# Performance work log

Hardware: AMD Instinct MI355X
Metric: run time of the kernel (lower is better)

## Reference

```python
import jax, jax.numpy as jnp
import numpy as np

E = 200000      # n_edges
IN = 128        # input_nf
HID = 32        # hidden_nf
H = 4           # att_heads
OUT = 128       # output_nf
MAXK = 16       # MAX_K neighbor slots


def setup_inputs() -> dict:
    key = jax.random.key(0)
    ks = jax.random.split(key, 12)
    Z = jax.random.normal(ks[0], (E, IN), dtype=jnp.float32)
    idx = jax.random.randint(ks[1], (E, 2, MAXK), 0, E)
    red = jax.random.uniform(ks[2], (E, 1, MAXK)) < 0.15
    klist = jnp.where(red, -1, idx).astype(jnp.int64)
    s = 0.05  # xavier-ish scale
    Wq = jax.random.normal(ks[3], (H, HID, IN), dtype=jnp.float32) * s
    Wk = jax.random.normal(ks[4], (H, HID, IN), dtype=jnp.float32) * s
    Wv = jax.random.normal(ks[5], (H, HID, IN), dtype=jnp.float32) * s
    Wb = jax.random.normal(ks[6], (H, 1, IN), dtype=jnp.float32) * s
    Wg = jax.random.normal(ks[7], (H, HID, IN), dtype=jnp.float32) * s
    bg = jnp.zeros((H, HID), dtype=jnp.float32)
    Wout = jax.random.normal(ks[8], (OUT, H * HID), dtype=jnp.float32) * s
    bout = jnp.zeros((OUT,), dtype=jnp.float32)
    return {"Z": Z, "klist": klist, "Wq": Wq, "Wk": Wk, "Wv": Wv,
            "Wb": Wb, "Wg": Wg, "bg": bg, "Wout": Wout, "bout": bout}


def reference(Z, klist, Wq, Wk, Wv, Wb, Wg, bg, Wout, bout):
    idx_i, idx_j = klist[:, 0], klist[:, 1]          # (E, K)
    red = idx_i == -1
    valid = (~red).astype(Z.dtype)[..., None]        # (E, K, 1)
    ii = jnp.where(red, 0, idx_i)
    jj = jnp.where(red, 0, idx_j)
    scale = 1.0 / np.sqrt(HID)
    outs = []
    for h in range(H):  # att_heads: small fixed loop over structurally distinct heads
        q = Z @ Wq[h].T                              # (E, HID)
        k = Z @ Wk[h].T
        v = Z @ Wv[h].T
        b = (Z @ Wb[h].T)[:, 0]                      # (E,)
        g = jax.nn.sigmoid(Z @ Wg[h].T + bg[h])      # (E, HID)
        tri_k = jnp.take(k, ii, axis=0) * valid      # (E, K, HID), redundant slots zeroed
        tri_v = jnp.take(v, ii, axis=0) * valid
        tri_b = jnp.take(b, jj, axis=0) * valid[..., 0]  # (E, K)
        scores = scale * jnp.einsum('eh,ekh->ek', q, tri_k) + tri_b
        alpha = jax.nn.softmax(scores, axis=1)       # (E, K)
        att = jnp.einsum('ek,ekh->eh', alpha, tri_v) # (E, HID)
        outs.append(g * att)
    out = jnp.concatenate(outs, axis=-1) @ Wout.T + bout  # (E, OUT)
    # dropout is identity in eval mode
    return out
```

## Files before the change

kernel.cpp:

```cpp
#include <hip/hip_runtime.h>
#include <hip/hip_bf16.h>
#include <stdint.h>

#define EDGES 200000
#define INF   128
#define HID   32
#define NHEAD 4
#define OUTF  128
#define MAXK  16

#define NPAD  528

#define XPAD  136

typedef unsigned short u16;
typedef __attribute__((ext_vector_type(8))) short bf16x8;
typedef __attribute__((ext_vector_type(4))) float f32x4;

__device__ __forceinline__ u16 f2bf(float f) {
  union { float f; uint32_t u; } v; v.f = f;
  uint32_t u = v.u;
  return (u16)((u + 0x7FFFu + ((u >> 16) & 1u)) >> 16);
}
__device__ __forceinline__ float bflo(uint32_t p) {
  union { uint32_t u; float f; } v; v.u = p << 16;
  return v.f;
}
__device__ __forceinline__ float bfhi(uint32_t p) {
  union { uint32_t u; float f; } v; v.u = p & 0xFFFF0000u;
  return v.f;
}

__device__ __forceinline__ uint32_t cvtpk_bf16(float lo, float hi) {
  float2 t; t.x = lo; t.y = hi;
  __hip_bfloat162 h = __float22bfloat162_rn(t);
  uint32_t u;
  __builtin_memcpy(&u, &h, 4);
  return u;
}
__device__ __forceinline__ bf16x8 pack8(float4 f0, float4 f1) {
  union { uint32_t u[4]; bf16x8 v; } r;
  r.u[0] = cvtpk_bf16(f0.x, f0.y);
  r.u[1] = cvtpk_bf16(f0.z, f0.w);
  r.u[2] = cvtpk_bf16(f1.x, f1.y);
  r.u[3] = cvtpk_bf16(f1.z, f1.w);
  return r.v;
}
__device__ __forceinline__ float sigm(float x) {
  return 1.0f / (1.0f + __expf(-x));
}

template <int CTRL>
__device__ __forceinline__ float dpp_add(float x) {
  int y = __builtin_amdgcn_update_dpp(0, __builtin_bit_cast(int, x),
                                      CTRL, 0xF, 0xF, true);
  return x + __builtin_bit_cast(float, y);
}
__device__ __forceinline__ float row16_sum(float x) {
  x = dpp_add<0xB1>(x);
  x = dpp_add<0x4E>(x);
  x = dpp_add<0x141>(x);
  x = dpp_add<0x140>(x);
  return x;
}

struct AccPair { f32x4 a, b; };
__device__ __forceinline__ AccPair tile_mm(const u16* __restrict__ W, int row0,
                                           int ml, int blk,
                                           const bf16x8 (&zfr)[2][4], int ldw) {
  bf16x8 wfr[4];
#pragma unroll
  for (int kk = 0; kk < 4; ++kk)
    wfr[kk] = *(const bf16x8*)(W + (size_t)(row0 + ml) * ldw + kk * 32 + blk * 8);
  AccPair r;
  r.a = (f32x4){0.f, 0.f, 0.f, 0.f};
  r.b = (f32x4){0.f, 0.f, 0.f, 0.f};
#pragma unroll
  for (int kk = 0; kk < 4; ++kk) {
    r.a = __builtin_amdgcn_mfma_f32_16x16x32_bf16(wfr[kk], zfr[0][kk], r.a, 0, 0, 0);
    r.b = __builtin_amdgcn_mfma_f32_16x16x32_bf16(wfr[kk], zfr[1][kk], r.b, 0, 0, 0);
  }
  return r;
}

__device__ __forceinline__ void ds_stage_pair(u16* sb, int ml, int blk, int t,
                                              uint2 pa, uint2 pb) {
  const int col2 = (t * 16 + blk * 4) * 2;
  const int swz = (ml & 7) << 4;
  *(uint2*)((char*)sb + ((ml * 128 + col2) ^ swz)) = pa;
  *(uint2*)((char*)sb + (((16 + ml) * 128 + col2) ^ swz)) = pb;
}
__device__ __forceinline__ void flush_group(const u16* sb, int lane,
                                            u16* __restrict__ dst, long e0,
                                            int rowu16, int colu16) {
  const int rr = lane >> 3;
  const int c8 = (lane & 7) * 8;
#pragma unroll
  for (int i = 0; i < 4; ++i) {
    const int row = i * 8 + rr;
    bf16x8 v = *(const bf16x8*)((const char*)sb +
                                ((row * 128 + c8 * 2) ^ ((row & 7) << 4)));
    *(bf16x8*)(dst + (e0 + row) * rowu16 + colu16 + c8) = v;
  }
}

__global__ __launch_bounds__(256) void prep_kernel(
    const float* __restrict__ Wq, const float* __restrict__ Wk,
    const float* __restrict__ Wv, const float* __restrict__ Wb,
    const float* __restrict__ Wg, const float* __restrict__ Wout,
    u16* __restrict__ Wc, u16* __restrict__ Woutb)
{
  int t = blockIdx.x * 256 + threadIdx.x;
  if (t < NPAD * INF) {
    int n = t >> 7, k = t & 127;
    float v = 0.0f;
    if (n < 128)       v = Wq[n * 128 + k];
    else if (n < 256)  v = Wg[(n - 128) * 128 + k];
    else if (n < 512) {
      int m = n - 256, h = m >> 6, c = m & 63;
      v = (c < 32) ? Wk[(h * 32 + c) * 128 + k] : Wv[(h * 32 + (c - 32)) * 128 + k];
    } else if (n < 516) v = Wb[(n - 512) * 128 + k];
    Wc[t] = f2bf(v);
  } else if (t < NPAD * INF + OUTF * 128) {
    int u = t - NPAD * INF;
    Woutb[u] = f2bf(Wout[u]);
  }
}

__global__ __launch_bounds__(256) void proj_kernel(
    const float* __restrict__ Z, const u16* __restrict__ Wc,
    const float* __restrict__ bg,
    u16* __restrict__ qb, u16* __restrict__ gb,
    u16* __restrict__ kvb, float* __restrict__ bb)
{
  __shared__ u16 stage[4][2][2048];

  const int wid = threadIdx.x >> 6, lane = threadIdx.x & 63;
  const int ml = lane & 15, blk = lane >> 4;
  const long e0 = (long)blockIdx.x * 128 + wid * 32;
  if (e0 >= EDGES) return;

  bf16x8 zfr[2][4];
#pragma unroll
  for (int s = 0; s < 2; ++s) {
    const float* zp = Z + (e0 + s * 16 + ml) * INF + blk * 8;
#pragma unroll
    for (int kk = 0; kk < 4; ++kk) {
      float4 f0 = *(const float4*)(zp + kk * 32);
      float4 f1 = *(const float4*)(zp + kk * 32 + 4);
      zfr[s][kk] = pack8(f0, f1);
    }
  }

  for (int g = 0; g < 2; ++g) {
    u16* sb = stage[wid][g & 1];
#pragma unroll
    for (int t = 0; t < 4; ++t) {
      AccPair acc = tile_mm(Wc, (g * 4 + t) * 16, ml, blk, zfr, INF);
      uint2 pa, pb;
      pa.x = cvtpk_bf16(acc.a[0], acc.a[1]); pa.y = cvtpk_bf16(acc.a[2], acc.a[3]);
      pb.x = cvtpk_bf16(acc.b[0], acc.b[1]); pb.y = cvtpk_bf16(acc.b[2], acc.b[3]);
      ds_stage_pair(sb, ml, blk, t, pa, pb);
    }
    flush_group(sb, lane, qb, e0, 128, g * 64);
  }

  for (int g = 0; g < 2; ++g) {
    u16* sb = stage[wid][g & 1];
#pragma unroll
    for (int t = 0; t < 4; ++t) {
      AccPair acc = tile_mm(Wc, (8 + g * 4 + t) * 16, ml, blk, zfr, INF);
      const int ng = g * 64 + t * 16 + blk * 4;
      float4 b4 = *(const float4*)(bg + ng);
      uint2 pa, pb;
      pa.x = cvtpk_bf16(sigm(acc.a[0] + b4.x), sigm(acc.a[1] + b4.y));
      pa.y = cvtpk_bf16(sigm(acc.a[2] + b4.z), sigm(acc.a[3] + b4.w));
      pb.x = cvtpk_bf16(sigm(acc.b[0] + b4.x), sigm(acc.b[1] + b4.y));
      pb.y = cvtpk_bf16(sigm(acc.b[2] + b4.z), sigm(acc.b[3] + b4.w));
      ds_stage_pair(sb, ml, blk, t, pa, pb);
    }
    flush_group(sb, lane, gb, e0, 128, g * 64);
  }

  for (int g = 0; g < 4; ++g) {
    u16* sb = stage[wid][g & 1];
#pragma unroll
    for (int t = 0; t < 4; ++t) {
      AccPair acc = tile_mm(Wc, (16 + g * 4 + t) * 16, ml, blk, zfr, INF);
      uint2 pa, pb;
      pa.x = cvtpk_bf16(acc.a[0], acc.a[1]); pa.y = cvtpk_bf16(acc.a[2], acc.a[3]);
      pb.x = cvtpk_bf16(acc.b[0], acc.b[1]); pb.y = cvtpk_bf16(acc.b[2], acc.b[3]);
      ds_stage_pair(sb, ml, blk, t, pa, pb);
    }
    flush_group(sb, lane, kvb, e0, 256, g * 64);
  }

  {
    AccPair acc = tile_mm(Wc, 512, ml, blk, zfr, INF);
    if (blk == 0) {
      *(float4*)(bb + (e0 + ml) * 4) =
          make_float4(acc.a[0], acc.a[1], acc.a[2], acc.a[3]);
      *(float4*)(bb + (e0 + 16 + ml) * 4) =
          make_float4(acc.b[0], acc.b[1], acc.b[2], acc.b[3]);
    }
  }
}

__global__ __launch_bounds__(256) void attn_out_kernel(
    const int* __restrict__ klist, const u16* __restrict__ qb,
    const u16* __restrict__ gb, const u16* __restrict__ kvb,
    const float* __restrict__ bb, const u16* __restrict__ Woutb,
    const float* __restrict__ bout, float* __restrict__ out)
{
  __shared__ u16 xs[32 * XPAD];

  const int wid = threadIdx.x >> 6;
  const int lane = threadIdx.x & 63;
  const long e0 = (long)blockIdx.x * 32;

  const int h = lane >> 4;
  const int kvo = h * 64 + (lane & 15) * 2;
  const float scale = 0.17677669529663687f;

#pragma unroll 1
  for (int it = 0; it < 8; ++it) {
    const int le = wid * 8 + it;
    int e = (int)e0 + le;
    e = __builtin_amdgcn_readfirstlane(e);

    const uint32_t q2 = *(const uint32_t*)(qb + (size_t)e * 128 + 2 * lane);
    const uint32_t g2 = *(const uint32_t*)(gb + (size_t)e * 128 + 2 * lane);
    const float q0 = bflo(q2), q1 = bfhi(q2);

    float sc[MAXK];
    uint32_t vvm[MAXK];
    const int* kl = klist + (size_t)e * 32;
#pragma unroll
    for (int nb = 0; nb < MAXK; ++nb) {
      const int ii = kl[nb];
      const int jj = kl[16 + nb];
      const bool valid = (ii >= 0);
      const int is = valid ? ii : 0;
      const int js = valid ? jj : 0;
      const u16* kvrow = kvb + (size_t)is * 256;
      uint32_t kki = *(const uint32_t*)(kvrow + kvo);
      uint32_t vvi = *(const uint32_t*)(kvrow + kvo + 32);
      float p = q0 * bflo(kki) + q1 * bfhi(kki);
      p = row16_sum(p);
      float bj = bb[(size_t)js * 4 + h];
      sc[nb]  = valid ? (scale * p + bj) : 0.0f;
      vvm[nb] = valid ? vvi : 0u;
    }

    float m = sc[0];
#pragma unroll
    for (int nb = 1; nb < MAXK; ++nb) m = fmaxf(m, sc[nb]);
    float s = 0.f, a0 = 0.f, a1 = 0.f;
#pragma unroll
    for (int nb = 0; nb < MAXK; ++nb) {
      float al = __expf(sc[nb] - m);
      s += al;
      a0 += al * bflo(vvm[nb]);
      a1 += al * bfhi(vvm[nb]);
    }
    float inv = 1.0f / s;
    uint32_t xo = cvtpk_bf16(bflo(g2) * a0 * inv, bfhi(g2) * a1 * inv);
    *(uint32_t*)(&xs[le * XPAD + 2 * lane]) = xo;
  }

  __syncthreads();

  const int ml = lane & 15, blk = lane >> 4;

  bf16x8 xfr[2][4];
#pragma unroll
  for (int s = 0; s < 2; ++s) {
#pragma unroll
    for (int kk = 0; kk < 4; ++kk)
      xfr[s][kk] = *(const bf16x8*)(&xs[(s * 16 + ml) * XPAD + kk * 32 + blk * 8]);
  }

  const long eA = e0 + ml, eB = e0 + 16 + ml;

#pragma unroll
  for (int t = 0; t < 2; ++t) {
    const int nt = wid * 2 + t;
    AccPair acc = tile_mm(Woutb, nt * 16, ml, blk, xfr, 128);
    const int o0 = nt * 16 + blk * 4;
    float4 b4 = *(const float4*)(bout + o0);
    float4 ra = make_float4(acc.a[0] + b4.x, acc.a[1] + b4.y,
                            acc.a[2] + b4.z, acc.a[3] + b4.w);
    float4 rb = make_float4(acc.b[0] + b4.x, acc.b[1] + b4.y,
                            acc.b[2] + b4.z, acc.b[3] + b4.w);
    *(float4*)(out + eA * 128 + o0) = ra;
    *(float4*)(out + eB * 128 + o0) = rb;
  }
}

extern "C" void kernel_launch(void* const* d_in, const int* in_sizes, int n_in,
                              void* d_out, int out_size, void* d_ws, size_t ws_size,
                              hipStream_t stream) {
  const float* Z     = (const float*)d_in[0];
  const int*   klist = (const int*)  d_in[1];
  const float* Wq    = (const float*)d_in[2];
  const float* Wk    = (const float*)d_in[3];
  const float* Wv    = (const float*)d_in[4];
  const float* Wb    = (const float*)d_in[5];
  const float* Wg    = (const float*)d_in[6];
  const float* bg    = (const float*)d_in[7];
  const float* Wout  = (const float*)d_in[8];
  const float* bout  = (const float*)d_in[9];
  float* out = (float*)d_out;

  char* ws = (char*)d_ws;
  u16*   Wc    = (u16*)(ws);
  u16*   Woutb = (u16*)(ws + 135168);
  u16*   qb    = (u16*)(ws + 167936);
  u16*   gb    = (u16*)(ws + 51367936);
  u16*   kvb   = (u16*)(ws + 102567936);
  float* bb    = (float*)(ws + 204967936);

  prep_kernel<<<(NPAD * INF + OUTF * 128 + 255) / 256, 256, 0, stream>>>(
      Wq, Wk, Wv, Wb, Wg, Wout, Wc, Woutb);
  proj_kernel<<<(EDGES + 127) / 128, 256, 0, stream>>>(
      Z, Wc, bg, qb, gb, kvb, bb);
  attn_out_kernel<<<EDGES / 32, 256, 0, stream>>>(
      klist, qb, gb, kvb, bb, Woutb, bout, out);
}
```

Measured before the change: 547.4 us.

## Compute q and gate projections inside attention kernel instead of global buffers

Moves the q and sigmoid-gate projections out of the projection kernel and into the attention kernel, which computes them per 32-edge block from Z via MFMA into shared memory. This removes writing and re-reading two bf16 E×128 intermediate buffers in global memory. In exchange, the attention kernel reads Z again (fp32, 512 B per edge), uses more LDS, which may lower occupancy, and adds a barrier before the gather phase.

```diff
diff --git a/kernel.cpp b/kernel.cpp
--- a/kernel.cpp
+++ b/kernel.cpp
@@ -81,6 +81,20 @@
     r.b = __builtin_amdgcn_mfma_f32_16x16x32_bf16(wfr[kk], zfr[1][kk], r.b, 0, 0, 0);
   }
   return r;
+}
+
+__device__ __forceinline__ void load_zfr(const float* __restrict__ Z, long e0,
+                                         int ml, int blk, bf16x8 (&zfr)[2][4]) {
+#pragma unroll
+  for (int s = 0; s < 2; ++s) {
+    const float* zp = Z + (e0 + s * 16 + ml) * INF + blk * 8;
+#pragma unroll
+    for (int kk = 0; kk < 4; ++kk) {
+      float4 f0 = *(const float4*)(zp + kk * 32);
+      float4 f1 = *(const float4*)(zp + kk * 32 + 4);
+      zfr[s][kk] = pack8(f0, f1);
+    }
+  }
 }
 
 __device__ __forceinline__ void ds_stage_pair(u16* sb, int ml, int blk, int t,
@@ -129,8 +143,6 @@
 
 __global__ __launch_bounds__(256) void proj_kernel(
     const float* __restrict__ Z, const u16* __restrict__ Wc,
-    const float* __restrict__ bg,
-    u16* __restrict__ qb, u16* __restrict__ gb,
     u16* __restrict__ kvb, float* __restrict__ bb)
 {
   __shared__ u16 stage[4][2][2048];
@@ -141,52 +153,13 @@
   if (e0 >= EDGES) return;
 
   bf16x8 zfr[2][4];
-#pragma unroll
-  for (int s = 0; s < 2; ++s) {
-    const float* zp = Z + (e0 + s * 16 + ml) * INF + blk * 8;
-#pragma unroll
-    for (int kk = 0; kk < 4; ++kk) {
-      float4 f0 = *(const float4*)(zp + kk * 32);
-      float4 f1 = *(const float4*)(zp + kk * 32 + 4);
-      zfr[s][kk] = pack8(f0, f1);
-    }
-  }
-
-  for (int g = 0; g < 2; ++g) {
-    u16* sb = stage[wid][g & 1];
-#pragma unroll
-    for (int t = 0; t < 4; ++t) {
-      AccPair acc = tile_mm(Wc, (g * 4 + t) * 16, ml, blk, zfr, INF);
-      uint2 pa, pb;
-      pa.x = cvtpk_bf16(acc.a[0], acc.a[1]); pa.y = cvtpk_bf16(acc.a[2], acc.a[3]);
-      pb.x = cvtpk_bf16(acc.b[0], acc.b[1]); pb.y = cvtpk_bf16(acc.b[2], acc.b[3]);
-      ds_stage_pair(sb, ml, blk, t, pa, pb);
-    }
-    flush_group(sb, lane, qb, e0, 128, g * 64);
-  }
-
-  for (int g = 0; g < 2; ++g) {
-    u16* sb = stage[wid][g & 1];
-#pragma unroll
-    for (int t = 0; t < 4; ++t) {
-      AccPair acc = tile_mm(Wc, (8 + g * 4 + t) * 16, ml, blk, zfr, INF);
-      const int ng = g * 64 + t * 16 + blk * 4;
-      float4 b4 = *(const float4*)(bg + ng);
-      uint2 pa, pb;
-      pa.x = cvtpk_bf16(sigm(acc.a[0] + b4.x), sigm(acc.a[1] + b4.y));
-      pa.y = cvtpk_bf16(sigm(acc.a[2] + b4.z), sigm(acc.a[3] + b4.w));
-      pb.x = cvtpk_bf16(sigm(acc.b[0] + b4.x), sigm(acc.b[1] + b4.y));
-      pb.y = cvtpk_bf16(sigm(acc.b[2] + b4.z), sigm(acc.b[3] + b4.w));
-      ds_stage_pair(sb, ml, blk, t, pa, pb);
-    }
-    flush_group(sb, lane, gb, e0, 128, g * 64);
-  }
+  load_zfr(Z, e0, ml, blk, zfr);
 
   for (int g = 0; g < 4; ++g) {
     u16* sb = stage[wid][g & 1];
 #pragma unroll
     for (int t = 0; t < 4; ++t) {
-      AccPair acc = tile_mm(Wc, (16 + g * 4 + t) * 16, ml, blk, zfr, INF);
+      AccPair acc = tile_mm(Wc, 256 + (g * 4 + t) * 16, ml, blk, zfr, INF);
       uint2 pa, pb;
       pa.x = cvtpk_bf16(acc.a[0], acc.a[1]); pa.y = cvtpk_bf16(acc.a[2], acc.a[3]);
       pb.x = cvtpk_bf16(acc.b[0], acc.b[1]); pb.y = cvtpk_bf16(acc.b[2], acc.b[3]);
@@ -207,16 +180,52 @@
 }
 
 __global__ __launch_bounds__(256) void attn_out_kernel(
-    const int* __restrict__ klist, const u16* __restrict__ qb,
-    const u16* __restrict__ gb, const u16* __restrict__ kvb,
+    const float* __restrict__ Z, const u16* __restrict__ Wc,
+    const float* __restrict__ bg,
+    const int* __restrict__ klist, const u16* __restrict__ kvb,
     const float* __restrict__ bb, const u16* __restrict__ Woutb,
     const float* __restrict__ bout, float* __restrict__ out)
 {
+  __shared__ u16 qs[32 * XPAD];
+  __shared__ u16 gs[32 * XPAD];
   __shared__ u16 xs[32 * XPAD];
 
   const int wid = threadIdx.x >> 6;
   const int lane = threadIdx.x & 63;
   const long e0 = (long)blockIdx.x * 32;
+  const int ml = lane & 15, blk = lane >> 4;
+
+  {
+    bf16x8 zfr[2][4];
+    load_zfr(Z, e0, ml, blk, zfr);
+
+#pragma unroll
+    for (int t = 0; t < 2; ++t) {
+      const int nt = wid * 2 + t;
+      AccPair acc = tile_mm(Wc, nt * 16, ml, blk, zfr, INF);
+      const int n0 = nt * 16 + blk * 4;
+      uint2 pa, pb;
+      pa.x = cvtpk_bf16(acc.a[0], acc.a[1]); pa.y = cvtpk_bf16(acc.a[2], acc.a[3]);
+      pb.x = cvtpk_bf16(acc.b[0], acc.b[1]); pb.y = cvtpk_bf16(acc.b[2], acc.b[3]);
+      *(uint2*)(&qs[ml * XPAD + n0]) = pa;
+      *(uint2*)(&qs[(16 + ml) * XPAD + n0]) = pb;
+    }
+#pragma unroll
+    for (int t = 0; t < 2; ++t) {
+      const int nt = wid * 2 + t;
+      AccPair acc = tile_mm(Wc, 128 + nt * 16, ml, blk, zfr, INF);
+      const int n0 = nt * 16 + blk * 4;
+      float4 b4 = *(const float4*)(bg + n0);
+      uint2 pa, pb;
+      pa.x = cvtpk_bf16(sigm(acc.a[0] + b4.x), sigm(acc.a[1] + b4.y));
+      pa.y = cvtpk_bf16(sigm(acc.a[2] + b4.z), sigm(acc.a[3] + b4.w));
+      pb.x = cvtpk_bf16(sigm(acc.b[0] + b4.x), sigm(acc.b[1] + b4.y));
+      pb.y = cvtpk_bf16(sigm(acc.b[2] + b4.z), sigm(acc.b[3] + b4.w));
+      *(uint2*)(&gs[ml * XPAD + n0]) = pa;
+      *(uint2*)(&gs[(16 + ml) * XPAD + n0]) = pb;
+    }
+  }
+  __syncthreads();
 
   const int h = lane >> 4;
   const int kvo = h * 64 + (lane & 15) * 2;
@@ -228,8 +237,8 @@
     int e = (int)e0 + le;
     e = __builtin_amdgcn_readfirstlane(e);
 
-    const uint32_t q2 = *(const uint32_t*)(qb + (size_t)e * 128 + 2 * lane);
-    const uint32_t g2 = *(const uint32_t*)(gb + (size_t)e * 128 + 2 * lane);
+    const uint32_t q2 = *(const uint32_t*)(&qs[le * XPAD + 2 * lane]);
+    const uint32_t g2 = *(const uint32_t*)(&gs[le * XPAD + 2 * lane]);
     const float q0 = bflo(q2), q1 = bfhi(q2);
 
     float sc[MAXK];
@@ -270,8 +279,6 @@
 
   __syncthreads();
 
-  const int ml = lane & 15, blk = lane >> 4;
-
   bf16x8 xfr[2][4];
 #pragma unroll
   for (int s = 0; s < 2; ++s) {
@@ -315,15 +322,13 @@
   char* ws = (char*)d_ws;
   u16*   Wc    = (u16*)(ws);
   u16*   Woutb = (u16*)(ws + 135168);
-  u16*   qb    = (u16*)(ws + 167936);
-  u16*   gb    = (u16*)(ws + 51367936);
-  u16*   kvb   = (u16*)(ws + 102567936);
-  float* bb    = (float*)(ws + 204967936);
+  u16*   kvb   = (u16*)(ws + 167936);
+  float* bb    = (float*)(ws + 102567936);
 
   prep_kernel<<<(NPAD * INF + OUTF * 128 + 255) / 256, 256, 0, stream>>>(
       Wq, Wk, Wv, Wb, Wg, Wout, Wc, Woutb);
   proj_kernel<<<(EDGES + 127) / 128, 256, 0, stream>>>(
-      Z, Wc, bg, qb, gb, kvb, bb);
+      Z, Wc, kvb, bb);
   attn_out_kernel<<<EDGES / 32, 256, 0, stream>>>(
-      klist, qb, gb, kvb, bb, Woutb, bout, out);
-}
+      Z, Wc, bg, klist, kvb, bb, Woutb, bout, out);
+}
```

Measured after the change: 516.6 us. 5.6% less time.
